# Optimization experiments

Measured on AMD Instinct MI355X. Metric: run time of the kernel, lower is better.

Reference implementation:

```python
import jax, jax.numpy as jnp
import numpy as np
import math

NUM_HEADS = 16

def _skew(QEr):
    # QEr: [B, H, S, S] -> pad 1 on left of last dim, reshape, drop first row
    B, H, S, _ = QEr.shape
    padded = jnp.pad(QEr, ((0, 0), (0, 0), (0, 0), (1, 0)))  # [B,H,S,S+1]
    reshaped = padded.reshape(B, H, S + 1, S)
    return reshaped[:, :, 1:, :]  # [B,H,S,S]

def setup_inputs() -> dict:
    key = jax.random.key(0)
    ks = jax.random.split(key, 8)
    B, S, D, dh = 4, 1024, 1024, 64
    x = jax.random.normal(ks[0], (B, S, D), dtype=jnp.float32)
    scale = 1.0 / math.sqrt(D)
    Wq = jax.random.normal(ks[1], (D, D), dtype=jnp.float32) * scale
    Wk = jax.random.normal(ks[2], (D, D), dtype=jnp.float32) * scale
    Wv = jax.random.normal(ks[3], (D, D), dtype=jnp.float32) * scale
    bq = jnp.zeros((D,), dtype=jnp.float32)
    bk = jnp.zeros((D,), dtype=jnp.float32)
    bv = jnp.zeros((D,), dtype=jnp.float32)
    Er = jax.random.normal(ks[4], (S, dh), dtype=jnp.float32)
    return {"x": x, "Wq": Wq, "bq": bq, "Wk": Wk, "bk": bk, "Wv": Wv, "bv": bv, "Er": Er}

def reference(x, Wq, bq, Wk, bk, Wv, bv, Er):
    B, S, D = x.shape
    H = NUM_HEADS
    dh = D // H
    # Linear projections (torch Linear: x @ W.T + b)
    q = (x @ Wq.T + bq).reshape(B, S, H, dh).transpose(0, 2, 1, 3)  # [B,H,S,dh]
    k = (x @ Wk.T + bk).reshape(B, S, H, dh).transpose(0, 2, 1, 3)
    v = (x @ Wv.T + bv).reshape(B, S, H, dh).transpose(0, 2, 1, 3)
    # Relative position term: q @ Er^T then skew (start = max_len - S = 0)
    QEr = jnp.einsum('bhsd,td->bhst', q, Er)  # [B,H,S,S]
    Srel = _skew(QEr)
    QKt = jnp.einsum('bhsd,bhtd->bhst', q, k)  # [B,H,S,S]
    attn = (QKt + Srel) / math.sqrt(dh)
    causal = jnp.tril(jnp.ones((S, S), dtype=bool))
    attn = jnp.where(causal[None, None], attn, jnp.float32(-1e6))
    attn = jax.nn.softmax(attn, axis=-1)
    out = jnp.einsum('bhst,bhtd->bhsd', attn, v)  # [B,H,S,dh]
    out = out.transpose(0, 2, 1, 3).reshape(B, S, D)
    return out  # dropout is identity in eval / p=0
```

## Files before the change

kernel.cpp:

```cpp
#include <hip/hip_runtime.h>
#include <stdint.h>

#define S_LEN 1024
#define DM 1024
#define NH 16
#define DH 64
#define NB 4

typedef unsigned short u16;
typedef __attribute__((ext_vector_type(8))) short short8;
typedef __attribute__((ext_vector_type(4))) float f32x4;
typedef __attribute__((ext_vector_type(4))) unsigned int u32x4;

__device__ __forceinline__ u16 f2bf(float f) {
  union { float f; unsigned int u; } c;
  c.f = f;
  unsigned int u = c.u;
  return (u16)((u + 0x7fffu + ((u >> 16) & 1u)) >> 16);
}

__device__ __forceinline__ void g2l16(const void* g, void* l) {
  __builtin_amdgcn_global_load_lds(
      (const __attribute__((address_space(1))) unsigned int*)(uintptr_t)g,
      (__attribute__((address_space(3))) unsigned int*)(uint32_t)(uintptr_t)l,
      16, 0, 0);
}

__global__ __launch_bounds__(256) void cvt_f32_bf16(
    const float* __restrict__ x, const float* __restrict__ Wq,
    const float* __restrict__ Wk, const float* __restrict__ Wv,
    const float* __restrict__ Er, u16* __restrict__ xb,
    u16* __restrict__ Wqb, u16* __restrict__ Wkb, u16* __restrict__ Wvb,
    u16* __restrict__ Erb) {
  const size_t f = ((size_t)blockIdx.x * 256 + threadIdx.x) * 8;
  const float* src;
  u16* dst;
  size_t off;
  if (f < 4194304) { src = x; dst = xb; off = f; }
  else if (f < 5242880) { src = Wq; dst = Wqb; off = f - 4194304; }
  else if (f < 6291456) { src = Wk; dst = Wkb; off = f - 5242880; }
  else if (f < 7340032) { src = Wv; dst = Wvb; off = f - 6291456; }
  else { src = Er; dst = Erb; off = f - 7340032; }
  const float4 a = *(const float4*)(src + off);
  const float4 b = *(const float4*)(src + off + 4);
  u16 o[8] = {f2bf(a.x), f2bf(a.y), f2bf(a.z), f2bf(a.w),
              f2bf(b.x), f2bf(b.y), f2bf(b.z), f2bf(b.w)};
  *(u32x4*)(dst + off) = *(const u32x4*)o;
}

__global__ __launch_bounds__(256) void qkv_gemm(
    const u16* __restrict__ x,
    const u16* __restrict__ Wq, const float* __restrict__ bq,
    const u16* __restrict__ Wk, const float* __restrict__ bk,
    const u16* __restrict__ Wv, const float* __restrict__ bv,
    u16* __restrict__ Qo, u16* __restrict__ Ko, u16* __restrict__ Vo) {
  __shared__ __attribute__((aligned(16))) u16 Al[128 * 32];
  __shared__ __attribute__((aligned(16))) u16 Bl[128 * 32];

  const int tid = threadIdx.x;
  const int lane = tid & 63;
  const int wave = tid >> 6;
  const int z = blockIdx.z;
  const u16* W = (z == 0) ? Wq : (z == 1) ? Wk : Wv;
  const float* bias = (z == 0) ? bq : (z == 1) ? bk : bv;

  const int m0 = blockIdx.y * 128;
  const int n0 = blockIdx.x * 128;

  f32x4 acc[4][4];
  const f32x4 fzero = {0.f, 0.f, 0.f, 0.f};
#pragma unroll
  for (int i = 0; i < 4; i++)
#pragma unroll
    for (int j = 0; j < 4; j++) acc[i][j] = fzero;

  const int srow = tid >> 2;
  const int schunk = tid & 3;
  const u16* gA = x + (size_t)(m0 + srow) * DM + schunk * 8;
  const u16* gB = W + (size_t)(n0 + srow) * DM + schunk * 8;

  const int fr = lane & 15;
  const int fq = lane >> 4;
  const int wr = (wave >> 1) * 64;
  const int wc = (wave & 1) * 64;

  for (int k = 0; k < DM; k += 32) {
    g2l16(gA + k, &Al[tid * 8]);
    g2l16(gA + (size_t)64 * DM + k, &Al[2048 + tid * 8]);
    g2l16(gB + k, &Bl[tid * 8]);
    g2l16(gB + (size_t)64 * DM + k, &Bl[2048 + tid * 8]);
    __syncthreads();
    short8 a[4], b[4];
#pragma unroll
    for (int i = 0; i < 4; i++)
      a[i] = *(const short8*)&Al[(wr + i * 16 + fr) * 32 + fq * 8];
#pragma unroll
    for (int j = 0; j < 4; j++)
      b[j] = *(const short8*)&Bl[(wc + j * 16 + fr) * 32 + fq * 8];
#pragma unroll
    for (int i = 0; i < 4; i++)
#pragma unroll
      for (int j = 0; j < 4; j++)
        acc[i][j] =
            __builtin_amdgcn_mfma_f32_16x16x32_bf16(a[i], b[j], acc[i][j], 0, 0, 0);
    __syncthreads();
  }

#pragma unroll
  for (int j = 0; j < 4; j++) {
    const int n = n0 + wc + j * 16 + fr;
    const float bsv = bias[n];
    const int h = n >> 6, d = n & (DH - 1);
#pragma unroll
    for (int i = 0; i < 4; i++) {
#pragma unroll
      for (int r = 0; r < 4; r++) {
        const int m = m0 + wr + i * 16 + fq * 4 + r;
        const int bb = m >> 10, s = m & (S_LEN - 1);
        const u16 o = f2bf(acc[i][j][r] + bsv);
        if (z == 2)
          Vo[((size_t)(bb * NH + h) * DH + d) * S_LEN + s] = o;
        else if (z == 1)
          Ko[((size_t)(bb * NH + h) * S_LEN + s) * DH + d] = o;
        else
          Qo[((size_t)(bb * NH + h) * S_LEN + s) * DH + d] = o;
      }
    }
  }
}

__device__ __forceinline__ f32x4 er_frag(const u16* __restrict__ Er, int e0,
                                         int fr, int fq, short8 aq0,
                                         short8 aq1) {
  int e = e0 + fr;
  e = (e > S_LEN - 1) ? (S_LEN - 1) : e;
  const short8 b0 = *(const short8*)&Er[(size_t)e * DH + fq * 8];
  const short8 b1 = *(const short8*)&Er[(size_t)e * DH + 32 + fq * 8];
  f32x4 z = {0.f, 0.f, 0.f, 0.f};
  z = __builtin_amdgcn_mfma_f32_16x16x32_bf16(aq0, b0, z, 0, 0, 0);
  z = __builtin_amdgcn_mfma_f32_16x16x32_bf16(aq1, b1, z, 0, 0, 0);
  return z;
}

__global__ __launch_bounds__(256, 4) void attn(
    const u16* __restrict__ Q, const u16* __restrict__ K,
    const u16* __restrict__ Vt, const u16* __restrict__ Er,
    float* __restrict__ out) {
  __shared__ __attribute__((aligned(16))) u16 Kl[2][64 * 64];
  __shared__ __attribute__((aligned(16))) u16 Vl[2][64 * 64];
  __shared__ __attribute__((aligned(16))) u16 Pl[4][16 * 64];

  const int tid = threadIdx.x;
  const int lane = tid & 63;
  const int w = tid >> 6;
  const int bh = blockIdx.y;
  const int b = bh >> 4, h = bh & (NH - 1);
  const int x = blockIdx.x;

  const u16* Qb = Q + (size_t)bh * S_LEN * DH;
  const char* Kb = (const char*)(K + (size_t)bh * S_LEN * DH);
  const char* Vb = (const char*)(Vt + (size_t)bh * DH * S_LEN);
  u16* Pw = Pl[w];

  const int fr = lane & 15;
  const int fq = lane >> 4;
  const f32x4 fzero = {0.f, 0.f, 0.f, 0.f};

  const int r0 = tid >> 3;
  const int ch = (tid & 7) * 16;

  auto stage = [&](int j0, int bf) {
#pragma unroll
    for (int q = 0; q < 2; q++) {
      const int row = q * 32 + r0;
      const int sw = ch ^ ((row & 7) << 4);
      g2l16(Kb + (size_t)(j0 + row) * 128 + sw,
            (char*)&Kl[bf][0] + row * 128 + ch);
      g2l16(Vb + (size_t)row * 2048 + j0 * 2 + sw,
            (char*)&Vl[bf][0] + row * 128 + ch);
    }
  };

  int buf = 0;
  stage(0, 0);
  __syncthreads();

  for (int half = 0; half < 2; half++) {
    const int a = half ? 15 - x : x;
    const int jmax = a * 64;
    const int i0w = a * 64 + w * 16;

    const short8 aq0 = *(const short8*)&Qb[(size_t)(i0w + fr) * DH + fq * 8];
    const short8 aq1 =
        *(const short8*)&Qb[(size_t)(i0w + fr) * DH + 32 + fq * 8];

    float mrow[4], lrow[4];
    f32x4 accO[4];
#pragma unroll
    for (int r = 0; r < 4; r++) { mrow[r] = -3.0e38f; lrow[r] = 0.f; }
#pragma unroll
    for (int t = 0; t < 4; t++) accO[t] = fzero;

    f32x4 zzc = fzero;

    for (int j0 = 0; j0 <= jmax; j0 += 64) {
      const int nj = (j0 < jmax) ? (j0 + 64) : (half == 0 ? 0 : -1);
      if (nj >= 0) stage(nj, buf ^ 1);

      const int tmax = (j0 == jmax) ? w : 3;
      const int eb = S_LEN - 16 - i0w + j0;

      const int ksw = (fr & 7) << 4;
      const char* Kbase = (const char*)&Kl[buf][0];
      f32x4 sfr[4];
#pragma unroll
      for (int t = 0; t < 4; t++) sfr[t] = fzero;
      __builtin_amdgcn_s_setprio(1);
#pragma unroll
      for (int t = 0; t < 4; t++)
        if (t <= tmax) {
          const char* kr = Kbase + (t * 16 + fr) * 128;
          const short8 b0 = *(const short8*)(kr + ((fq * 16) ^ ksw));
          const short8 b1 = *(const short8*)(kr + ((64 + fq * 16) ^ ksw));
          f32x4 z = fzero;
          z = __builtin_amdgcn_mfma_f32_16x16x32_bf16(aq0, b0, z, 0, 0, 0);
          z = __builtin_amdgcn_mfma_f32_16x16x32_bf16(aq1, b1, z, 0, 0, 0);
          sfr[t] = z;
        }
      __builtin_amdgcn_s_setprio(0);

      f32x4 zz[5];
#pragma unroll
      for (int f = 0; f < 5; f++) zz[f] = fzero;
      if (j0 > 0) zz[0] = zzc;
      const int f0 = (j0 == 0) ? 0 : 1;
#pragma unroll
      for (int f = 0; f < 5; f++)
        if (f >= f0 && f <= tmax + 1)
          zz[f] = er_frag(Er, eb + f * 16, fr, fq, aq0, aq1);
      zzc = zz[4];

      float p[4][4];
#pragma unroll
      for (int r = 0; r < 4; r++) {
        const int row = fq * 4 + r;
        const int c = 15 - row + fr;
        const int src = (fq << 4) | (c & 15);
        float sh[5];
#pragma unroll
        for (int f = 0; f < 5; f++) sh[f] = __shfl(zz[f][r], src);
#pragma unroll
        for (int t = 0; t < 4; t++) {
          const float rel = (c < 16) ? sh[t] : sh[t + 1];
          float sv = (sfr[t][r] + rel) * 0.125f;
          const int jj = j0 + t * 16 + fr;
          const int ii = i0w + row;
          if (jj > ii) sv = -3.0e38f;
          p[t][r] = sv;
        }
      }

#pragma unroll
      for (int r = 0; r < 4; r++) {
        float rm = fmaxf(fmaxf(p[0][r], p[1][r]), fmaxf(p[2][r], p[3][r]));
#pragma unroll
        for (int off = 1; off < 16; off <<= 1)
          rm = fmaxf(rm, __shfl_xor(rm, off));
        const float mnew = fmaxf(mrow[r], rm);
        const float alpha = __expf(mrow[r] - mnew);
        mrow[r] = mnew;
        float rs = 0.f;
#pragma unroll
        for (int t = 0; t < 4; t++) {
          const float e = __expf(p[t][r] - mnew);
          p[t][r] = e;
          rs += e;
        }
#pragma unroll
        for (int off = 1; off < 16; off <<= 1) rs += __shfl_xor(rs, off);
        lrow[r] = lrow[r] * alpha + rs;
#pragma unroll
        for (int t = 0; t < 4; t++) accO[t][r] *= alpha;
      }

#pragma unroll
      for (int t = 0; t < 4; t++)
#pragma unroll
        for (int r = 0; r < 4; r++)
          Pw[(fq * 4 + r) * 64 + (((t ^ fq) << 4) + fr)] = f2bf(p[t][r]);
      __builtin_amdgcn_s_waitcnt(0xC07F);

      const int rsw = (fr >> 2) << 4;
      const short8 ap0 = *(const short8*)&Pw[fr * 64 + ((fq * 8) ^ rsw)];
      const short8 ap1 = *(const short8*)&Pw[fr * 64 + ((32 + fq * 8) ^ rsw)];

      const char* Vbase = (const char*)&Vl[buf][0];
      __builtin_amdgcn_s_setprio(1);
#pragma unroll
      for (int t = 0; t < 4; t++) {
        const char* vr = Vbase + (t * 16 + fr) * 128;
        const short8 b0 = *(const short8*)(vr + ((fq * 16) ^ ksw));
        const short8 b1 = *(const short8*)(vr + ((64 + fq * 16) ^ ksw));
        accO[t] =
            __builtin_amdgcn_mfma_f32_16x16x32_bf16(ap0, b0, accO[t], 0, 0, 0);
        accO[t] =
            __builtin_amdgcn_mfma_f32_16x16x32_bf16(ap1, b1, accO[t], 0, 0, 0);
      }
      __builtin_amdgcn_s_setprio(0);

      __syncthreads();
      buf ^= 1;
    }

#pragma unroll
    for (int r = 0; r < 4; r++) {
      const float inv = 1.f / lrow[r];
      const int s = i0w + fq * 4 + r;
#pragma unroll
      for (int t = 0; t < 4; t++) {
        const int d = t * 16 + fr;
        out[((size_t)b * S_LEN + s) * DM + h * DH + d] = accO[t][r] * inv;
      }
    }
  }
}

extern "C" void kernel_launch(void* const* d_in, const int* in_sizes, int n_in,
                              void* d_out, int out_size, void* d_ws, size_t ws_size,
                              hipStream_t stream) {
  const float* x = (const float*)d_in[0];
  const float* Wq = (const float*)d_in[1];
  const float* bq = (const float*)d_in[2];
  const float* Wk = (const float*)d_in[3];
  const float* bk = (const float*)d_in[4];
  const float* Wv = (const float*)d_in[5];
  const float* bv = (const float*)d_in[6];
  const float* Er = (const float*)d_in[7];
  float* out = (float*)d_out;

  const size_t per = (size_t)NB * NH * S_LEN * DH;
  u16* Qw = (u16*)d_ws;
  u16* Kw = Qw + per;
  u16* Vw = Kw + per;
  u16* xb = Vw + per;
  u16* Wqb = xb + per;
  u16* Wkb = Wqb + (size_t)DM * DM;
  u16* Wvb = Wkb + (size_t)DM * DM;
  u16* Erb = Wvb + (size_t)DM * DM;

  cvt_f32_bf16<<<3616, 256, 0, stream>>>(x, Wq, Wk, Wv, Er, xb, Wqb, Wkb, Wvb,
                                         Erb);
  dim3 g1(DM / 128, (NB * S_LEN) / 128, 3);
  qkv_gemm<<<g1, dim3(256), 0, stream>>>(xb, Wqb, bq, Wkb, bk, Wvb, bv, Qw, Kw,
                                         Vw);
  dim3 g2(8, NB * NH);
  attn<<<g2, dim3(256), 0, stream>>>(Qw, Kw, Vw, Erb, out);
}
```

Measured before the change: 191.9 us.

## Use 8-wave attention blocks over 128-row query tiles and DPP row reductions

Each attention block previously paired two 64-row query tiles, processed one after the other. It now launches 512 threads (8 waves) covering a single 128-row query tile, so each K/V tile staged into LDS is shared by twice as many waves. Load balancing now comes from reversing the tile index for the second half of the batch-heads rather than pairing tiles inside a block. Row max and sum reductions now use DPP intrinsics instead of shuffle-xor loops. The costs are a single barrier across eight waves, idle waves on the diagonal tiles, and more register and occupancy pressure per block.

Result: no change. 188.5 us (-1.8%).

```diff
diff --git a/kernel.cpp b/kernel.cpp
--- a/kernel.cpp
+++ b/kernel.cpp
@@ -24,6 +24,31 @@
       (const __attribute__((address_space(1))) unsigned int*)(uintptr_t)g,
       (__attribute__((address_space(3))) unsigned int*)(uint32_t)(uintptr_t)l,
       16, 0, 0);
+}
+
+__device__ __forceinline__ float grp16_max(float v) {
+  union { float f; int i; } c, o;
+  c.f = v; o.i = __builtin_amdgcn_update_dpp(c.i, c.i, 0xB1, 0xF, 0xF, false);
+  v = fmaxf(v, o.f);
+  c.f = v; o.i = __builtin_amdgcn_update_dpp(c.i, c.i, 0x4E, 0xF, 0xF, false);
+  v = fmaxf(v, o.f);
+  c.f = v; o.i = __builtin_amdgcn_update_dpp(c.i, c.i, 0x124, 0xF, 0xF, false);
+  v = fmaxf(v, o.f);
+  c.f = v; o.i = __builtin_amdgcn_update_dpp(c.i, c.i, 0x128, 0xF, 0xF, false);
+  v = fmaxf(v, o.f);
+  return v;
+}
+__device__ __forceinline__ float grp16_sum(float v) {
+  union { float f; int i; } c, o;
+  c.f = v; o.i = __builtin_amdgcn_update_dpp(c.i, c.i, 0xB1, 0xF, 0xF, false);
+  v += o.f;
+  c.f = v; o.i = __builtin_amdgcn_update_dpp(c.i, c.i, 0x4E, 0xF, 0xF, false);
+  v += o.f;
+  c.f = v; o.i = __builtin_amdgcn_update_dpp(c.i, c.i, 0x124, 0xF, 0xF, false);
+  v += o.f;
+  c.f = v; o.i = __builtin_amdgcn_update_dpp(c.i, c.i, 0x128, 0xF, 0xF, false);
+  v += o.f;
+  return v;
 }
 
 __global__ __launch_bounds__(256) void cvt_f32_bf16(
@@ -142,20 +167,22 @@
   return z;
 }
 
-__global__ __launch_bounds__(256, 4) void attn(
+__global__ __launch_bounds__(512, 4) void attn(
     const u16* __restrict__ Q, const u16* __restrict__ K,
     const u16* __restrict__ Vt, const u16* __restrict__ Er,
     float* __restrict__ out) {
   __shared__ __attribute__((aligned(16))) u16 Kl[2][64 * 64];
   __shared__ __attribute__((aligned(16))) u16 Vl[2][64 * 64];
-  __shared__ __attribute__((aligned(16))) u16 Pl[4][16 * 64];
+  __shared__ __attribute__((aligned(16))) u16 Pl[8][16 * 64];
 
   const int tid = threadIdx.x;
   const int lane = tid & 63;
   const int w = tid >> 6;
   const int bh = blockIdx.y;
   const int b = bh >> 4, h = bh & (NH - 1);
-  const int x = blockIdx.x;
+  const int it = (bh < 32) ? (int)blockIdx.x : 7 - (int)blockIdx.x;
+  const int i0 = it * 128;
+  const int jmax = i0 + 64;
 
   const u16* Qb = Q + (size_t)bh * S_LEN * DH;
   const char* Kb = (const char*)(K + (size_t)bh * S_LEN * DH);
@@ -168,50 +195,42 @@
 
   const int r0 = tid >> 3;
   const int ch = (tid & 7) * 16;
+  const int sw = ch ^ ((r0 & 7) << 4);
 
   auto stage = [&](int j0, int bf) {
-#pragma unroll
-    for (int q = 0; q < 2; q++) {
-      const int row = q * 32 + r0;
-      const int sw = ch ^ ((row & 7) << 4);
-      g2l16(Kb + (size_t)(j0 + row) * 128 + sw,
-            (char*)&Kl[bf][0] + row * 128 + ch);
-      g2l16(Vb + (size_t)row * 2048 + j0 * 2 + sw,
-            (char*)&Vl[bf][0] + row * 128 + ch);
-    }
+    g2l16(Kb + (size_t)(j0 + r0) * 128 + sw,
+          (char*)&Kl[bf][0] + r0 * 128 + ch);
+    g2l16(Vb + (size_t)r0 * 2048 + j0 * 2 + sw,
+          (char*)&Vl[bf][0] + r0 * 128 + ch);
   };
+
+  const int i0w = i0 + w * 16;
+  const short8 aq0 = *(const short8*)&Qb[(size_t)(i0w + fr) * DH + fq * 8];
+  const short8 aq1 = *(const short8*)&Qb[(size_t)(i0w + fr) * DH + 32 + fq * 8];
+
+  float mrow[4], lrow[4];
+  f32x4 accO[4];
+#pragma unroll
+  for (int r = 0; r < 4; r++) { mrow[r] = -3.0e38f; lrow[r] = 0.f; }
+#pragma unroll
+  for (int t = 0; t < 4; t++) accO[t] = fzero;
+
+  f32x4 zzc = fzero;
 
   int buf = 0;
   stage(0, 0);
   __syncthreads();
 
-  for (int half = 0; half < 2; half++) {
-    const int a = half ? 15 - x : x;
-    const int jmax = a * 64;
-    const int i0w = a * 64 + w * 16;
-
-    const short8 aq0 = *(const short8*)&Qb[(size_t)(i0w + fr) * DH + fq * 8];
-    const short8 aq1 =
-        *(const short8*)&Qb[(size_t)(i0w + fr) * DH + 32 + fq * 8];
-
-    float mrow[4], lrow[4];
-    f32x4 accO[4];
-#pragma unroll
-    for (int r = 0; r < 4; r++) { mrow[r] = -3.0e38f; lrow[r] = 0.f; }
-#pragma unroll
-    for (int t = 0; t < 4; t++) accO[t] = fzero;
-
-    f32x4 zzc = fzero;
-
-    for (int j0 = 0; j0 <= jmax; j0 += 64) {
-      const int nj = (j0 < jmax) ? (j0 + 64) : (half == 0 ? 0 : -1);
-      if (nj >= 0) stage(nj, buf ^ 1);
-
-      const int tmax = (j0 == jmax) ? w : 3;
-      const int eb = S_LEN - 16 - i0w + j0;
-
+  for (int j0 = 0; j0 <= jmax; j0 += 64) {
+    if (j0 < jmax) stage(j0 + 64, buf ^ 1);
+
+    int tmax = (i0w + 15 - j0) >> 4;
+    if (tmax > 3) tmax = 3;
+
+    if (tmax >= 0) {
       const int ksw = (fr & 7) << 4;
       const char* Kbase = (const char*)&Kl[buf][0];
+
       f32x4 sfr[4];
 #pragma unroll
       for (int t = 0; t < 4; t++) sfr[t] = fzero;
@@ -229,15 +248,16 @@
         }
       __builtin_amdgcn_s_setprio(0);
 
+      const int eb = S_LEN - 16 - i0w + j0;
       f32x4 zz[5];
 #pragma unroll
       for (int f = 0; f < 5; f++) zz[f] = fzero;
-      if (j0 > 0) zz[0] = zzc;
       const int f0 = (j0 == 0) ? 0 : 1;
 #pragma unroll
       for (int f = 0; f < 5; f++)
         if (f >= f0 && f <= tmax + 1)
           zz[f] = er_frag(Er, eb + f * 16, fr, fq, aq0, aq1);
+      if (j0 > 0) zz[0] = zzc;
       zzc = zz[4];
 
       float p[4][4];
@@ -263,9 +283,7 @@
 #pragma unroll
       for (int r = 0; r < 4; r++) {
         float rm = fmaxf(fmaxf(p[0][r], p[1][r]), fmaxf(p[2][r], p[3][r]));
-#pragma unroll
-        for (int off = 1; off < 16; off <<= 1)
-          rm = fmaxf(rm, __shfl_xor(rm, off));
+        rm = grp16_max(rm);
         const float mnew = fmaxf(mrow[r], rm);
         const float alpha = __expf(mrow[r] - mnew);
         mrow[r] = mnew;
@@ -276,8 +294,7 @@
           p[t][r] = e;
           rs += e;
         }
-#pragma unroll
-        for (int off = 1; off < 16; off <<= 1) rs += __shfl_xor(rs, off);
+        rs = grp16_sum(rs);
         lrow[r] = lrow[r] * alpha + rs;
 #pragma unroll
         for (int t = 0; t < 4; t++) accO[t][r] *= alpha;
@@ -307,20 +324,20 @@
             __builtin_amdgcn_mfma_f32_16x16x32_bf16(ap1, b1, accO[t], 0, 0, 0);
       }
       __builtin_amdgcn_s_setprio(0);
-
-      __syncthreads();
-      buf ^= 1;
     }
 
-#pragma unroll
-    for (int r = 0; r < 4; r++) {
-      const float inv = 1.f / lrow[r];
-      const int s = i0w + fq * 4 + r;
-#pragma unroll
-      for (int t = 0; t < 4; t++) {
-        const int d = t * 16 + fr;
-        out[((size_t)b * S_LEN + s) * DM + h * DH + d] = accO[t][r] * inv;
-      }
+    __syncthreads();
+    buf ^= 1;
+  }
+
+#pragma unroll
+  for (int r = 0; r < 4; r++) {
+    const float inv = 1.f / lrow[r];
+    const int s = i0w + fq * 4 + r;
+#pragma unroll
+    for (int t = 0; t < 4; t++) {
+      const int d = t * 16 + fr;
+      out[((size_t)b * S_LEN + s) * DM + h * DH + d] = accO[t][r] * inv;
     }
   }
 }
@@ -354,5 +371,5 @@
   qkv_gemm<<<g1, dim3(256), 0, stream>>>(xb, Wqb, bq, Wkb, bk, Wvb, bv, Qw, Kw,
                                          Vw);
   dim3 g2(8, NB * NH);
-  attn<<<g2, dim3(256), 0, stream>>>(Qw, Kw, Vw, Erb, out);
-}
+  attn<<<g2, dim3(512), 0, stream>>>(Qw, Kw, Vw, Erb, out);
+}
```
